# Performance work log

Measured on AMD Instinct MI355X. Metric: run time of the kernel, lower is better.

Reference implementation:

```python
import jax, jax.numpy as jnp
import numpy as np

H = 16          # num_heads
TOP_K = 2
LN_EPS = 1e-5


def setup_inputs() -> dict:
    key = jax.random.key(0)
    ks = jax.random.split(key, 8)
    B, S, E, NE = 2, 1024, 1024, 8
    w = lambda k, shp: jax.random.normal(k, shp, dtype=jnp.float32) * 0.02
    return {
        "x": jax.random.normal(ks[0], (B, S, E), dtype=jnp.float32),
        "rW1": w(ks[1], (E // 2, E)),
        "rb1": jnp.zeros((E // 2,), jnp.float32),
        "ln_g": jnp.ones((E // 2,), jnp.float32),
        "ln_b": jnp.zeros((E // 2,), jnp.float32),
        "rW2": w(ks[2], (NE, E // 2)),
        "rb2": jnp.zeros((NE,), jnp.float32),
        "qW": w(ks[3], (NE, E, E)),
        "qb": jnp.zeros((NE, E), jnp.float32),
        "kW": w(ks[4], (NE, E, E)),
        "kb": jnp.zeros((NE, E), jnp.float32),
        "vW": w(ks[5], (NE, E, E)),
        "vb": jnp.zeros((NE, E), jnp.float32),
        "oW": w(ks[6], (NE, E, E)),
        "ob": jnp.zeros((NE, E), jnp.float32),
    }


def reference(x, rW1, rb1, ln_g, ln_b, rW2, rb2, qW, qb, kW, kb, vW, vb, oW, ob):
    B, S, E = x.shape
    NE = qW.shape[0]
    Dh = E // H
    scale = 1.0 / jnp.sqrt(jnp.asarray(Dh, x.dtype))

    # ---- router: Linear -> LayerNorm -> ReLU -> Linear ----
    h = x @ rW1.T + rb1                       # [B,S,E/2]
    mu = h.mean(-1, keepdims=True)
    var = ((h - mu) ** 2).mean(-1, keepdims=True)
    h = (h - mu) * jax.lax.rsqrt(var + LN_EPS) * ln_g + ln_b
    h = jax.nn.relu(h)
    logits = h @ rW2.T + rb2                  # [B,S,NE]
    probs = jax.nn.softmax(logits, axis=-1)

    # ---- top-k gating, renormalized, scattered to dense expert mask ----
    tp, ti = jax.lax.top_k(probs, TOP_K)      # [B,S,K]
    tp = tp / tp.sum(-1, keepdims=True)
    expert_mask = (jax.nn.one_hot(ti, NE, dtype=probs.dtype) * tp[..., None]).sum(-2)  # [B,S,NE]
    gates = jnp.moveaxis(expert_mask, -1, 0)  # [NE,B,S]

    # ---- every expert attends over all tokens; outputs gated and summed ----
    def expert_step(acc, params):
        qw, qb_, kw, kb_, vw, vb_, ow, ob_, g = params
        q = (x @ qw.T + qb_).reshape(B, S, H, Dh).transpose(0, 2, 1, 3)  # [B,H,S,Dh]
        k = (x @ kw.T + kb_).reshape(B, S, H, Dh).transpose(0, 2, 1, 3)
        v = (x @ vw.T + vb_).reshape(B, S, H, Dh).transpose(0, 2, 1, 3)
        scores = jnp.einsum("bhqd,bhkd->bhqk", q, k) * scale
        p = jax.nn.softmax(scores, axis=-1)
        o = jnp.einsum("bhqk,bhkd->bhqd", p, v)
        o = o.transpose(0, 2, 1, 3).reshape(B, S, E) @ ow.T + ob_
        return acc + o * g[..., None], None

    out, _ = jax.lax.scan(expert_step, jnp.zeros_like(x),
                          (qW, qb, kW, kb, vW, vb, oW, ob, gates))
    return out
```

## Files before the change

### kernel.cpp

```cpp
#include <hip/hip_runtime.h>
#include <hip/hip_bf16.h>

typedef unsigned short u16;
typedef unsigned int u32;
typedef __bf16 bf16x8 __attribute__((ext_vector_type(8)));
typedef float f32x4 __attribute__((ext_vector_type(4)));

__device__ __forceinline__ u16 f2bf(float f) {
  union { float f; unsigned u; } v; v.f = f;
  unsigned r = v.u + 0x7fffu + ((v.u >> 16) & 1u);
  return (u16)(r >> 16);
}

__device__ __forceinline__ f32x4 mfma16(bf16x8 a, bf16x8 b, f32x4 c) {
  return __builtin_amdgcn_mfma_f32_16x16x32_bf16(a, b, c, 0, 0, 0);
}

__device__ __forceinline__ void gl_lds16(const u16* g, u16* l) {
  __builtin_amdgcn_global_load_lds(
      (const __attribute__((address_space(1))) u32*)g,
      (__attribute__((address_space(3))) u32*)l, 16, 0, 0);
}

__global__ __launch_bounds__(256) void cvt_x_kernel(const float* __restrict__ x, u16* __restrict__ xb) {
  size_t i = (size_t)blockIdx.x * 256 + threadIdx.x;
  float4 v = reinterpret_cast<const float4*>(x)[i];
  unsigned long long pk = (unsigned long long)f2bf(v.x) |
                          ((unsigned long long)f2bf(v.y) << 16) |
                          ((unsigned long long)f2bf(v.z) << 32) |
                          ((unsigned long long)f2bf(v.w) << 48);
  *reinterpret_cast<unsigned long long*>(xb + i * 4) = pk;
}

__global__ __launch_bounds__(256) void cvt_w_kernel(
    const float* __restrict__ qW, const float* __restrict__ kW,
    const float* __restrict__ vW, const float* __restrict__ oW,
    u16* __restrict__ wb_qkv, u16* __restrict__ wb_o) {
  const size_t nqkv4 = (size_t)8 * 3 * 262144;
  const size_t total = nqkv4 + (size_t)8 * 262144;
  for (size_t i = (size_t)blockIdx.x * 256 + threadIdx.x; i < total;
       i += (size_t)gridDim.x * 256) {
    const float* src; u16* dst;
    if (i < nqkv4) {
      size_t elem = i * 4;
      size_t blk = elem >> 20;
      size_t el = blk / 3, ty = blk % 3;
      const float* W = (ty == 0 ? qW : (ty == 1 ? kW : vW));
      src = W + el * 1048576 + (elem & 1048575);
      dst = wb_qkv + elem;
    } else {
      size_t elem = (i - nqkv4) * 4;
      size_t el = elem >> 20;
      src = oW + el * 1048576 + (elem & 1048575);
      dst = wb_o + elem;
    }
    float4 v = *reinterpret_cast<const float4*>(src);
    unsigned long long pk = (unsigned long long)f2bf(v.x) |
                            ((unsigned long long)f2bf(v.y) << 16) |
                            ((unsigned long long)f2bf(v.z) << 32) |
                            ((unsigned long long)f2bf(v.w) << 48);
    *reinterpret_cast<unsigned long long*>(dst) = pk;
  }
}

__global__ __launch_bounds__(256) void zero_lists(u32* __restrict__ lists) {
  int i = blockIdx.x * 256 + threadIdx.x;
  if (i < 32784) lists[i] = 0;
}

__global__ __launch_bounds__(256) void router_gemm1(
    const float* __restrict__ x, const float* __restrict__ rW1,
    const float* __restrict__ rb1, float* __restrict__ hbuf) {
  __shared__ float aT[16][72];
  __shared__ float bT[16][72];
  int t = threadIdx.x;
  int tx = t & 15, ty = t >> 4;
  int m0 = blockIdx.x * 64, n0 = blockIdx.y * 64;
  float acc[4][4];
#pragma unroll
  for (int i = 0; i < 4; ++i)
#pragma unroll
    for (int j = 0; j < 4; ++j) acc[i][j] = 0.f;
  const float* Ab = x + (size_t)m0 * 1024;
  const float* Bb = rW1 + (size_t)n0 * 1024;
  int r = t >> 2, c4 = (t & 3) * 4;
  for (int k0 = 0; k0 < 1024; k0 += 16) {
    float4 av = *reinterpret_cast<const float4*>(Ab + (size_t)r * 1024 + k0 + c4);
    float4 bv = *reinterpret_cast<const float4*>(Bb + (size_t)r * 1024 + k0 + c4);
    aT[c4 + 0][r] = av.x; aT[c4 + 1][r] = av.y; aT[c4 + 2][r] = av.z; aT[c4 + 3][r] = av.w;
    bT[c4 + 0][r] = bv.x; bT[c4 + 1][r] = bv.y; bT[c4 + 2][r] = bv.z; bT[c4 + 3][r] = bv.w;
    __syncthreads();
#pragma unroll
    for (int kk = 0; kk < 16; ++kk) {
      float4 a = *reinterpret_cast<const float4*>(&aT[kk][ty * 4]);
      float4 b = *reinterpret_cast<const float4*>(&bT[kk][tx * 4]);
      float aa[4] = {a.x, a.y, a.z, a.w};
      float bb[4] = {b.x, b.y, b.z, b.w};
#pragma unroll
      for (int i = 0; i < 4; ++i)
#pragma unroll
        for (int j = 0; j < 4; ++j) acc[i][j] += aa[i] * bb[j];
    }
    __syncthreads();
  }
#pragma unroll
  for (int i = 0; i < 4; ++i) {
    int row = m0 + ty * 4 + i;
#pragma unroll
    for (int j = 0; j < 4; ++j) {
      int col = n0 + tx * 4 + j;
      hbuf[(size_t)row * 512 + col] = acc[i][j] + rb1[col];
    }
  }
}

__global__ __launch_bounds__(64) void router_finish(
    const float* __restrict__ hbuf, const float* __restrict__ ln_g,
    const float* __restrict__ ln_b, const float* __restrict__ rW2,
    const float* __restrict__ rb2,
    u32* __restrict__ tok_list, float* __restrict__ gate_list,
    u32* __restrict__ cnt, u32* __restrict__ inv) {
  int tok = blockIdx.x, lane = threadIdx.x;
  const float* hr = hbuf + (size_t)tok * 512;
  float4 v0 = *reinterpret_cast<const float4*>(hr + lane * 8);
  float4 v1 = *reinterpret_cast<const float4*>(hr + lane * 8 + 4);
  float hv[8] = {v0.x, v0.y, v0.z, v0.w, v1.x, v1.y, v1.z, v1.w};
  float s = 0.f;
#pragma unroll
  for (int j = 0; j < 8; ++j) s += hv[j];
#pragma unroll
  for (int m = 1; m < 64; m <<= 1) s += __shfl_xor(s, m);
  float mu = s * (1.0f / 512.0f);
  float s2 = 0.f;
#pragma unroll
  for (int j = 0; j < 8; ++j) { float d = hv[j] - mu; s2 += d * d; }
#pragma unroll
  for (int m = 1; m < 64; m <<= 1) s2 += __shfl_xor(s2, m);
  float rstd = 1.0f / sqrtf(s2 * (1.0f / 512.0f) + 1e-5f);
#pragma unroll
  for (int j = 0; j < 8; ++j) {
    float tv = (hv[j] - mu) * rstd * ln_g[lane * 8 + j] + ln_b[lane * 8 + j];
    hv[j] = fmaxf(tv, 0.0f);
  }
  float logit[8];
#pragma unroll
  for (int n = 0; n < 8; ++n) {
    const float* wr = rW2 + (size_t)n * 512 + lane * 8;
    float p = 0.f;
#pragma unroll
    for (int j = 0; j < 8; ++j) p += hv[j] * wr[j];
#pragma unroll
    for (int m = 1; m < 64; m <<= 1) p += __shfl_xor(p, m);
    logit[n] = p + rb2[n];
  }
  int i1 = 0; float l1 = logit[0];
#pragma unroll
  for (int n = 1; n < 8; ++n) if (logit[n] > l1) { l1 = logit[n]; i1 = n; }
  int i2 = -1; float l2 = -3.4e38f;
#pragma unroll
  for (int n = 0; n < 8; ++n) if (n != i1 && logit[n] > l2) { l2 = logit[n]; i2 = n; }
  float e2 = __expf(l2 - l1);
  float g1 = 1.0f / (1.0f + e2);
  float g2 = e2 * g1;
  if (lane == 0) {
    int b = tok >> 10, sq = tok & 1023;
    int p1 = i1 * 2 + b;
    u32 pos1 = atomicAdd(&cnt[p1], 1u);
    tok_list[p1 * 1024 + pos1] = (u32)sq;
    gate_list[p1 * 1024 + pos1] = g1;
    inv[tok * 2 + 0] = ((u32)p1 << 10) | pos1;
    int p2 = i2 * 2 + b;
    u32 pos2 = atomicAdd(&cnt[p2], 1u);
    tok_list[p2 * 1024 + pos2] = (u32)sq;
    gate_list[p2 * 1024 + pos2] = g2;
    inv[tok * 2 + 1] = ((u32)p2 << 10) | pos2;
  }
}

__device__ __forceinline__ void stage8(
    const u16* aS0, const u16* aS1, const u16* aS2, const u16* aS3,
    const u16* bS0, const u16* bS1, const u16* bS2, const u16* bS3,
    int k0, u16* aL, u16* bL, int w) {
  gl_lds16(aS0 + k0, aL + (32 * w + 0) * 64);
  gl_lds16(aS1 + k0, aL + (32 * w + 8) * 64);
  gl_lds16(aS2 + k0, aL + (32 * w + 16) * 64);
  gl_lds16(aS3 + k0, aL + (32 * w + 24) * 64);
  gl_lds16(bS0 + k0, bL + (32 * w + 0) * 64);
  gl_lds16(bS1 + k0, bL + (32 * w + 8) * 64);
  gl_lds16(bS2 + k0, bL + (32 * w + 16) * 64);
  gl_lds16(bS3 + k0, bL + (32 * w + 24) * 64);
}

__device__ __forceinline__ void gemm_mainloop_p(
    const u16* aS0, const u16* aS1, const u16* aS2, const u16* aS3,
    const u16* bS0, const u16* bS1, const u16* bS2, const u16* bS3,
    int K, u16* aL0, u16* bL0, u16* aL1, u16* bL1, f32x4 acc[4][4]) {
  const int t = threadIdx.x;
  const int w = t >> 6, lane = t & 63;
  const int wm = (w >> 1) * 64, wn = (w & 1) * 64;
  const int lr = lane & 15, lg = lane >> 4;
  const int T = K >> 6;
  stage8(aS0, aS1, aS2, aS3, bS0, bS1, bS2, bS3, 0, aL0, bL0, w);
  __syncthreads();
  for (int tt = 0; tt < T; ++tt) {
    u16* aC = (tt & 1) ? aL1 : aL0;
    u16* bC = (tt & 1) ? bL1 : bL0;
    if (tt + 1 < T) {
      u16* aN = (tt & 1) ? aL0 : aL1;
      u16* bN = (tt & 1) ? bL0 : bL1;
      stage8(aS0, aS1, aS2, aS3, bS0, bS1, bS2, bS3, (tt + 1) << 6, aN, bN, w);
    }
    __builtin_amdgcn_s_setprio(1);
#pragma unroll
    for (int kk = 0; kk < 2; ++kk) {
      bf16x8 af[4], bfr[4];
#pragma unroll
      for (int i = 0; i < 4; ++i) {
        int ra = wm + i * 16 + lr;
        af[i] = *reinterpret_cast<const bf16x8*>(aC + ra * 64 + (((kk * 4 + lg) ^ (ra & 7)) << 3));
        int rb = wn + i * 16 + lr;
        bfr[i] = *reinterpret_cast<const bf16x8*>(bC + rb * 64 + (((kk * 4 + lg) ^ (rb & 7)) << 3));
      }
#pragma unroll
      for (int mi = 0; mi < 4; ++mi)
#pragma unroll
        for (int ni = 0; ni < 4; ++ni)
          acc[mi][ni] = mfma16(af[mi], bfr[ni], acc[mi][ni]);
    }
    __builtin_amdgcn_s_setprio(0);
    __syncthreads();
  }
}

__global__ __launch_bounds__(256) void kv_gemm_kernel(
    const u16* __restrict__ xb, const u16* __restrict__ wb_qkv,
    const float* __restrict__ kb, const float* __restrict__ vb,
    u16* __restrict__ kvbuf) {
  __shared__ u16 lds[32768];
  int orig = blockIdx.x;
  int wgid = (orig & 7) * 256 + (orig >> 3);
  int nblk = wgid & 7, mblk = (wgid >> 3) & 15;
  int ty = (wgid >> 7) & 1, e = wgid >> 8;
  const int t = threadIdx.x, w = t >> 6, lane = t & 63;
  const int rloc = lane >> 3, cloc = lane & 7;
  const int sc8 = (cloc ^ rloc) * 8;
  const u16* A = xb + (size_t)mblk * 128 * 1024;
  const u16* B = wb_qkv + (size_t)(e * 3 + 1 + ty) * 1048576 + (size_t)nblk * 128 * 1024;
  f32x4 acc[4][4];
#pragma unroll
  for (int i = 0; i < 4; ++i)
#pragma unroll
    for (int j = 0; j < 4; ++j) { f32x4 z = {0.f, 0.f, 0.f, 0.f}; acc[i][j] = z; }
  gemm_mainloop_p(
      A + (size_t)(32 * w + 0 + rloc) * 1024 + sc8, A + (size_t)(32 * w + 8 + rloc) * 1024 + sc8,
      A + (size_t)(32 * w + 16 + rloc) * 1024 + sc8, A + (size_t)(32 * w + 24 + rloc) * 1024 + sc8,
      B + (size_t)(32 * w + 0 + rloc) * 1024 + sc8, B + (size_t)(32 * w + 8 + rloc) * 1024 + sc8,
      B + (size_t)(32 * w + 16 + rloc) * 1024 + sc8, B + (size_t)(32 * w + 24 + rloc) * 1024 + sc8,
      1024, lds, lds + 8192, lds + 16384, lds + 24576, acc);
  const int wm = (w >> 1) * 64, wn = (w & 1) * 64;
  const int lr = lane & 15, lg = lane >> 4;
  const float* bias = (ty ? vb : kb) + (size_t)e * 1024 + nblk * 128;
  u16* Cb = kvbuf + ((size_t)(e * 2 + ty) * 2048 + (size_t)mblk * 128) * 1024 + nblk * 128;
#pragma unroll
  for (int ni = 0; ni < 4; ++ni) {
    int lcol = wn + ni * 16 + lr;
    float bv = bias[lcol];
#pragma unroll
    for (int mi = 0; mi < 4; ++mi)
#pragma unroll
      for (int rg = 0; rg < 4; ++rg) {
        int lrow = wm + mi * 16 + lg * 4 + rg;
        Cb[(size_t)lrow * 1024 + lcol] = f2bf(acc[mi][ni][rg] + bv);
      }
  }
}

__global__ __launch_bounds__(256) void q_gemm_kernel(
    const u16* __restrict__ xb, const u16* __restrict__ wb_qkv,
    const float* __restrict__ qb, const u32* __restrict__ tok_list,
    const u32* __restrict__ cnt, u16* __restrict__ qc) {
  __shared__ u16 lds[32768];
  int nblk = blockIdx.x, mt = blockIdx.y, p = blockIdx.z;
  int c = (int)cnt[p];
  if (mt * 128 >= c) return;
  int e = p >> 1, b = p & 1;
  const int t = threadIdx.x, w = t >> 6, lane = t & 63;
  const int rloc = lane >> 3, cloc = lane & 7;
  const int sc8 = (cloc ^ rloc) * 8;
  const u32* tl = tok_list + p * 1024 + mt * 128 + 32 * w + rloc;
  int t0 = (int)(tl[0] & 1023), t1 = (int)(tl[8] & 1023);
  int t2 = (int)(tl[16] & 1023), t3 = (int)(tl[24] & 1023);
  const u16* Ab = xb + (size_t)b * 1024 * 1024 + sc8;
  const u16* B = wb_qkv + (size_t)(e * 3) * 1048576 + (size_t)nblk * 128 * 1024;
  f32x4 acc[4][4];
#pragma unroll
  for (int i = 0; i < 4; ++i)
#pragma unroll
    for (int j = 0; j < 4; ++j) { f32x4 z = {0.f, 0.f, 0.f, 0.f}; acc[i][j] = z; }
  gemm_mainloop_p(
      Ab + (size_t)t0 * 1024, Ab + (size_t)t1 * 1024, Ab + (size_t)t2 * 1024, Ab + (size_t)t3 * 1024,
      B + (size_t)(32 * w + 0 + rloc) * 1024 + sc8, B + (size_t)(32 * w + 8 + rloc) * 1024 + sc8,
      B + (size_t)(32 * w + 16 + rloc) * 1024 + sc8, B + (size_t)(32 * w + 24 + rloc) * 1024 + sc8,
      1024, lds, lds + 8192, lds + 16384, lds + 24576, acc);
  const int wm = (w >> 1) * 64, wn = (w & 1) * 64;
  const int lr = lane & 15, lg = lane >> 4;
  const float* bias = qb + (size_t)e * 1024 + nblk * 128;
  u16* Cb = qc + ((size_t)p * 1024 + (size_t)mt * 128) * 1024 + nblk * 128;
#pragma unroll
  for (int ni = 0; ni < 4; ++ni) {
    int lcol = wn + ni * 16 + lr;
    float bv = bias[lcol];
#pragma unroll
    for (int mi = 0; mi < 4; ++mi)
#pragma unroll
      for (int rg = 0; rg < 4; ++rg) {
        int lrow = wm + mi * 16 + lg * 4 + rg;
        Cb[(size_t)lrow * 1024 + lcol] = f2bf(acc[mi][ni][rg] + bv);
      }
  }
}

__global__ __launch_bounds__(256) void attn_kernel(
    const u16* __restrict__ qc, const u16* __restrict__ kvbuf,
    const u32* __restrict__ cnt, u16* __restrict__ oc) {
  __shared__ u16 Kl[4096];
  __shared__ u32 Vtl[2048];
  __shared__ u16 Pl[4096];
  int h = blockIdx.x;
  int p = blockIdx.y >> 3, lt = blockIdx.y & 7;
  int c = (int)cnt[p];
  if (lt * 64 >= c) return;
  int e = p >> 1, b = p & 1;
  const u16* Qb = qc + ((size_t)p * 1024 + (size_t)lt * 64) * 1024 + h * 64;
  const u16* Kg = kvbuf + ((size_t)(e * 2 + 0) * 2048 + (size_t)b * 1024) * 1024 + h * 64;
  const u16* Vg = kvbuf + ((size_t)(e * 2 + 1) * 2048 + (size_t)b * 1024) * 1024 + h * 64;
  u16* Og = oc + ((size_t)p * 1024 + (size_t)lt * 64) * 1024 + h * 64;
  const int t = threadIdx.x, w = t >> 6, lane = t & 63;
  const int lr = lane & 15, lg = lane >> 4;
  const int krow_l = lane >> 3, kc = lane & 7;
  const int s2 = t >> 3, sc3 = t & 7;

  bf16x8 qa0 = *reinterpret_cast<const bf16x8*>(Qb + (size_t)(w * 16 + lr) * 1024 + lg * 8);
  bf16x8 qa1 = *reinterpret_cast<const bf16x8*>(Qb + (size_t)(w * 16 + lr) * 1024 + 32 + lg * 8);

  f32x4 oacc[4];
  float mrun[4], lsum[4];
#pragma unroll
  for (int i = 0; i < 4; ++i) {
    f32x4 z = {0.f, 0.f, 0.f, 0.f}; oacc[i] = z; mrun[i] = -3.4e38f; lsum[i] = 0.f;
  }

  for (int it = 0; it < 16; ++it) {
    int kv0 = it * 64;
#pragma unroll
    for (int r = 0; r < 2; ++r) {
      int row = 16 * w + 8 * r + krow_l;
      gl_lds16(Kg + (size_t)(kv0 + row) * 1024 + (kc ^ (row & 7)) * 8,
               Kl + (16 * w + 8 * r) * 64);
    }
    {
      int4 v0r = *reinterpret_cast<const int4*>(Vg + (size_t)(kv0 + 2 * s2) * 1024 + sc3 * 8);
      int4 v1r = *reinterpret_cast<const int4*>(Vg + (size_t)(kv0 + 2 * s2 + 1) * 1024 + sc3 * 8);
      const u16* v0 = reinterpret_cast<const u16*>(&v0r);
      const u16* v1 = reinterpret_cast<const u16*>(&v1r);
#pragma unroll
      for (int j = 0; j < 8; ++j) {
        int jj = (j + sc3) & 7;
        int d = sc3 * 8 + jj;
        u32 val = (u32)v0[jj] | ((u32)v1[jj] << 16);
        Vtl[d * 32 + (((s2 >> 2) ^ (d & 7)) << 2) + (s2 & 3)] = val;
      }
    }
    __syncthreads();
    f32x4 sv[4];
    __builtin_amdgcn_s_setprio(1);
#pragma unroll
    for (int nt = 0; nt < 4; ++nt) {
      f32x4 z = {0.f, 0.f, 0.f, 0.f};
#pragma unroll
      for (int kk = 0; kk < 2; ++kk) {
        int rk = nt * 16 + lr;
        bf16x8 kf = *reinterpret_cast<const bf16x8*>(Kl + rk * 64 + (((kk * 4 + lg) ^ (rk & 7)) << 3));
        z = mfma16(kk ? qa1 : qa0, kf, z);
      }
      sv[nt] = z * 0.125f;
    }
    __builtin_amdgcn_s_setprio(0);
#pragma unroll
    for (int rg = 0; rg < 4; ++rg) {
      float tm = fmaxf(fmaxf(sv[0][rg], sv[1][rg]), fmaxf(sv[2][rg], sv[3][rg]));
#pragma unroll
      for (int mm = 1; mm < 16; mm <<= 1) tm = fmaxf(tm, __shfl_xor(tm, mm));
      float mn = fmaxf(mrun[rg], tm);
      float al = __expf(mrun[rg] - mn);
      mrun[rg] = mn;
      lsum[rg] *= al;
#pragma unroll
      for (int nt = 0; nt < 4; ++nt) oacc[nt][rg] *= al;
    }
#pragma unroll
    for (int nt = 0; nt < 4; ++nt) {
#pragma unroll
      for (int rg = 0; rg < 4; ++rg) {
        float pv = __expf(sv[nt][rg] - mrun[rg]);
        lsum[rg] += pv;
        int prow = lg * 4 + rg;
        Pl[w * 1024 + prow * 64 + ((nt * 16 + lr) ^ ((prow & 7) << 3))] = f2bf(pv);
      }
    }
    __builtin_amdgcn_s_setprio(1);
#pragma unroll
    for (int kk = 0; kk < 2; ++kk) {
      bf16x8 pf = *reinterpret_cast<const bf16x8*>(
          Pl + w * 1024 + lr * 64 + (((kk * 4 + lg) ^ (lr & 7)) << 3));
#pragma unroll
      for (int nt = 0; nt < 4; ++nt) {
        int rv = nt * 16 + lr;
        bf16x8 vf = *reinterpret_cast<const bf16x8*>(
            reinterpret_cast<const u16*>(Vtl) + rv * 64 + (((kk * 4 + lg) ^ (rv & 7)) << 3));
        oacc[nt] = mfma16(pf, vf, oacc[nt]);
      }
    }
    __builtin_amdgcn_s_setprio(0);
    __syncthreads();
  }
#pragma unroll
  for (int rg = 0; rg < 4; ++rg) {
#pragma unroll
    for (int mm = 1; mm < 16; mm <<= 1) lsum[rg] += __shfl_xor(lsum[rg], mm);
    float inv = 1.0f / lsum[rg];
#pragma unroll
    for (int nt = 0; nt < 4; ++nt)
      Og[(size_t)(w * 16 + lg * 4 + rg) * 1024 + nt * 16 + lr] = f2bf(oacc[nt][rg] * inv);
  }
}

__global__ __launch_bounds__(256) void oproj_kernel(
    const u16* __restrict__ oc, const u16* __restrict__ wb_o,
    const u32* __restrict__ cnt, float* __restrict__ projc) {
  __shared__ u16 lds[32768];
  int nblk = blockIdx.x, mt = blockIdx.y, p = blockIdx.z;
  int c = (int)cnt[p];
  if (mt * 128 >= c) return;
  int e = p >> 1;
  const int t = threadIdx.x, w = t >> 6, lane = t & 63;
  const int rloc = lane >> 3, cloc = lane & 7;
  const int sc8 = (cloc ^ rloc) * 8;
  const u16* A = oc + ((size_t)p * 1024 + (size_t)mt * 128) * 1024;
  const u16* B = wb_o + (size_t)e * 1048576 + (size_t)nblk * 128 * 1024;
  f32x4 acc[4][4];
#pragma unroll
  for (int i = 0; i < 4; ++i)
#pragma unroll
    for (int j = 0; j < 4; ++j) { f32x4 z = {0.f, 0.f, 0.f, 0.f}; acc[i][j] = z; }
  gemm_mainloop_p(
      A + (size_t)(32 * w + 0 + rloc) * 1024 + sc8, A + (size_t)(32 * w + 8 + rloc) * 1024 + sc8,
      A + (size_t)(32 * w + 16 + rloc) * 1024 + sc8, A + (size_t)(32 * w + 24 + rloc) * 1024 + sc8,
      B + (size_t)(32 * w + 0 + rloc) * 1024 + sc8, B + (size_t)(32 * w + 8 + rloc) * 1024 + sc8,
      B + (size_t)(32 * w + 16 + rloc) * 1024 + sc8, B + (size_t)(32 * w + 24 + rloc) * 1024 + sc8,
      1024, lds, lds + 8192, lds + 16384, lds + 24576, acc);
  const int wm = (w >> 1) * 64, wn = (w & 1) * 64;
  const int lr = lane & 15, lg = lane >> 4;
  float* Pb = projc + ((size_t)p * 1024 + (size_t)mt * 128) * 1024 + nblk * 128;
#pragma unroll
  for (int mi = 0; mi < 4; ++mi)
#pragma unroll
    for (int rg = 0; rg < 4; ++rg) {
      int lrow = wm + mi * 16 + lg * 4 + rg;
#pragma unroll
      for (int ni = 0; ni < 4; ++ni) {
        int lcol = wn + ni * 16 + lr;
        Pb[(size_t)lrow * 1024 + lcol] = acc[mi][ni][rg];
      }
    }
}

__global__ __launch_bounds__(256) void merge_out(
    const float* __restrict__ projc, const float* __restrict__ ob,
    const float* __restrict__ gate_list, const u32* __restrict__ inv,
    float* __restrict__ out) {
  int tok = blockIdx.x;
  int c4 = threadIdx.x * 4;
  u32 i1 = inv[tok * 2], i2 = inv[tok * 2 + 1];
  int idx1 = (int)(i1 >> 10) * 1024 + (int)(i1 & 1023);
  int idx2 = (int)(i2 >> 10) * 1024 + (int)(i2 & 1023);
  float g1 = gate_list[idx1], g2 = gate_list[idx2];
  int e1 = (int)(i1 >> 11), e2 = (int)(i2 >> 11);
  float4 a = *reinterpret_cast<const float4*>(projc + (size_t)idx1 * 1024 + c4);
  float4 bvec = *reinterpret_cast<const float4*>(projc + (size_t)idx2 * 1024 + c4);
  float4 o1 = *reinterpret_cast<const float4*>(ob + (size_t)e1 * 1024 + c4);
  float4 o2 = *reinterpret_cast<const float4*>(ob + (size_t)e2 * 1024 + c4);
  float4 r;
  r.x = g1 * (a.x + o1.x) + g2 * (bvec.x + o2.x);
  r.y = g1 * (a.y + o1.y) + g2 * (bvec.y + o2.y);
  r.z = g1 * (a.z + o1.z) + g2 * (bvec.z + o2.z);
  r.w = g1 * (a.w + o1.w) + g2 * (bvec.w + o2.w);
  *reinterpret_cast<float4*>(out + (size_t)tok * 1024 + c4) = r;
}

extern "C" void kernel_launch(void* const* d_in, const int* in_sizes, int n_in,
                              void* d_out, int out_size, void* d_ws, size_t ws_size,
                              hipStream_t stream) {
  const float* x    = (const float*)d_in[0];
  const float* rW1  = (const float*)d_in[1];
  const float* rb1  = (const float*)d_in[2];
  const float* ln_g = (const float*)d_in[3];
  const float* ln_b = (const float*)d_in[4];
  const float* rW2  = (const float*)d_in[5];
  const float* rb2  = (const float*)d_in[6];
  const float* qW   = (const float*)d_in[7];
  const float* qb   = (const float*)d_in[8];
  const float* kW   = (const float*)d_in[9];
  const float* kb   = (const float*)d_in[10];
  const float* vW   = (const float*)d_in[11];
  const float* vb   = (const float*)d_in[12];
  const float* oW   = (const float*)d_in[13];
  const float* ob   = (const float*)d_in[14];
  float* out = (float*)d_out;

  const size_t need = 50331648ull + 16777216ull + 67108864ull + 33554432ull +
                      33554432ull + 4194304ull + 147520ull;
  if (ws_size < need) return;
  char* pp = (char*)d_ws;
  u16* wb_qkv = (u16*)pp; pp += 50331648ull;
  u16* wb_o   = (u16*)pp; pp += 16777216ull;
  u16* kvbuf  = (u16*)pp; pp += 67108864ull;
  u16* qc     = (u16*)pp; pp += 33554432ull;
  u16* oc     = (u16*)pp; pp += 33554432ull;
  u16* xb     = (u16*)pp; pp += 4194304ull;
  u32* lists  = (u32*)pp;
  u32* tok_list    = lists;
  float* gate_list = (float*)(lists + 16384);
  u32* cnt         = lists + 32768;
  u32* inv         = lists + 32784;
  float* hbuf  = (float*)qc;
  float* projc = (float*)kvbuf;

  cvt_x_kernel<<<dim3(2048), dim3(256), 0, stream>>>(x, xb);
  cvt_w_kernel<<<dim3(2048), dim3(256), 0, stream>>>(qW, kW, vW, oW, wb_qkv, wb_o);
  router_gemm1<<<dim3(32, 8), dim3(256), 0, stream>>>(x, rW1, rb1, hbuf);
  zero_lists<<<dim3(129), dim3(256), 0, stream>>>(lists);
  router_finish<<<dim3(2048), dim3(64), 0, stream>>>(hbuf, ln_g, ln_b, rW2, rb2,
                                                     tok_list, gate_list, cnt, inv);
  kv_gemm_kernel<<<dim3(2048), dim3(256), 0, stream>>>(xb, wb_qkv, kb, vb, kvbuf);
  q_gemm_kernel<<<dim3(8, 8, 16), dim3(256), 0, stream>>>(xb, wb_qkv, qb, tok_list, cnt, qc);
  attn_kernel<<<dim3(16, 128), dim3(256), 0, stream>>>(qc, kvbuf, cnt, oc);
  oproj_kernel<<<dim3(8, 8, 16), dim3(256), 0, stream>>>(oc, wb_o, cnt, projc);
  merge_out<<<dim3(2048), dim3(256), 0, stream>>>(projc, ob, gate_list, inv, out);
}
```

Before: 539.5 us.

## Emit transposed V from the KV GEMM and double-buffer K/V tiles in attention

The V projection GEMM now swaps its operands (weight times x) so it writes V already transposed per expert and batch into a separate buffer. K also moves to its own buffer. The attention kernel can then stage both K and V^T tiles with direct global-to-LDS loads, instead of doing register-level V transposes with scattered LDS stores. It also double-buffers these tiles, prefetching the next KV block while computing the current one. The cost is twice the K/V LDS footprint, a per-row bias lookup in the V epilogue, and reliance on the existing end-of-loop barrier to order the async LDS loads.

Result: faster. 485.3 us (-10.0%).

```diff
diff --git a/kernel.cpp b/kernel.cpp
--- a/kernel.cpp
+++ b/kernel.cpp
@@ -235,17 +235,26 @@
 __global__ __launch_bounds__(256) void kv_gemm_kernel(
     const u16* __restrict__ xb, const u16* __restrict__ wb_qkv,
     const float* __restrict__ kb, const float* __restrict__ vb,
-    u16* __restrict__ kvbuf) {
+    u16* __restrict__ kbuf, u16* __restrict__ vtbuf) {
   __shared__ u16 lds[32768];
   int orig = blockIdx.x;
   int wgid = (orig & 7) * 256 + (orig >> 3);
-  int nblk = wgid & 7, mblk = (wgid >> 3) & 15;
-  int ty = (wgid >> 7) & 1, e = wgid >> 8;
+  int e = wgid >> 8, r = wgid & 255;
+  int ty = r >> 7, rr = r & 127;
   const int t = threadIdx.x, w = t >> 6, lane = t & 63;
   const int rloc = lane >> 3, cloc = lane & 7;
   const int sc8 = (cloc ^ rloc) * 8;
-  const u16* A = xb + (size_t)mblk * 128 * 1024;
-  const u16* B = wb_qkv + (size_t)(e * 3 + 1 + ty) * 1048576 + (size_t)nblk * 128 * 1024;
+  const u16 *A, *B;
+  int mblk, nblk;
+  if (ty == 0) {
+    mblk = rr >> 3; nblk = rr & 7;
+    A = xb + (size_t)mblk * 128 * 1024;
+    B = wb_qkv + (size_t)(e * 3 + 1) * 1048576 + (size_t)nblk * 128 * 1024;
+  } else {
+    mblk = rr & 7; nblk = rr >> 3;
+    A = wb_qkv + (size_t)(e * 3 + 2) * 1048576 + (size_t)mblk * 128 * 1024;
+    B = xb + (size_t)nblk * 128 * 1024;
+  }
   f32x4 acc[4][4];
 #pragma unroll
   for (int i = 0; i < 4; ++i)
@@ -259,19 +268,36 @@
       1024, lds, lds + 8192, lds + 16384, lds + 24576, acc);
   const int wm = (w >> 1) * 64, wn = (w & 1) * 64;
   const int lr = lane & 15, lg = lane >> 4;
-  const float* bias = (ty ? vb : kb) + (size_t)e * 1024 + nblk * 128;
-  u16* Cb = kvbuf + ((size_t)(e * 2 + ty) * 2048 + (size_t)mblk * 128) * 1024 + nblk * 128;
-#pragma unroll
-  for (int ni = 0; ni < 4; ++ni) {
-    int lcol = wn + ni * 16 + lr;
-    float bv = bias[lcol];
-#pragma unroll
-    for (int mi = 0; mi < 4; ++mi)
-#pragma unroll
-      for (int rg = 0; rg < 4; ++rg) {
-        int lrow = wm + mi * 16 + lg * 4 + rg;
-        Cb[(size_t)lrow * 1024 + lcol] = f2bf(acc[mi][ni][rg] + bv);
-      }
+  if (ty == 0) {
+    const float* bias = kb + (size_t)e * 1024 + nblk * 128;
+    u16* Cb = kbuf + ((size_t)e * 2048 + (size_t)mblk * 128) * 1024 + nblk * 128;
+#pragma unroll
+    for (int ni = 0; ni < 4; ++ni) {
+      int lcol = wn + ni * 16 + lr;
+      float bv = bias[lcol];
+#pragma unroll
+      for (int mi = 0; mi < 4; ++mi)
+#pragma unroll
+        for (int rg = 0; rg < 4; ++rg) {
+          int lrow = wm + mi * 16 + lg * 4 + rg;
+          Cb[(size_t)lrow * 1024 + lcol] = f2bf(acc[mi][ni][rg] + bv);
+        }
+    }
+  } else {
+    const float* bias = vb + (size_t)e * 1024 + mblk * 128;
+    int bb = nblk >> 3, nn = nblk & 7;
+    u16* Cb = vtbuf + ((size_t)(e * 2 + bb) * 1024 + (size_t)mblk * 128) * 1024 + nn * 128;
+#pragma unroll
+    for (int ni = 0; ni < 4; ++ni) {
+      int lcol = wn + ni * 16 + lr;
+#pragma unroll
+      for (int mi = 0; mi < 4; ++mi)
+#pragma unroll
+        for (int rg = 0; rg < 4; ++rg) {
+          int lrow = wm + mi * 16 + lg * 4 + rg;
+          Cb[(size_t)lrow * 1024 + lcol] = f2bf(acc[mi][ni][rg] + bias[lrow]);
+        }
+    }
   }
 }
 
@@ -321,10 +347,11 @@
 }
 
 __global__ __launch_bounds__(256) void attn_kernel(
-    const u16* __restrict__ qc, const u16* __restrict__ kvbuf,
-    const u32* __restrict__ cnt, u16* __restrict__ oc) {
-  __shared__ u16 Kl[4096];
-  __shared__ u32 Vtl[2048];
+    const u16* __restrict__ qc, const u16* __restrict__ kbuf,
+    const u16* __restrict__ vtbuf, const u32* __restrict__ cnt,
+    u16* __restrict__ oc) {
+  __shared__ u16 Kl[2][4096];
+  __shared__ u16 Vtl[2][4096];
   __shared__ u16 Pl[4096];
   int h = blockIdx.x;
   int p = blockIdx.y >> 3, lt = blockIdx.y & 7;
@@ -332,13 +359,27 @@
   if (lt * 64 >= c) return;
   int e = p >> 1, b = p & 1;
   const u16* Qb = qc + ((size_t)p * 1024 + (size_t)lt * 64) * 1024 + h * 64;
-  const u16* Kg = kvbuf + ((size_t)(e * 2 + 0) * 2048 + (size_t)b * 1024) * 1024 + h * 64;
-  const u16* Vg = kvbuf + ((size_t)(e * 2 + 1) * 2048 + (size_t)b * 1024) * 1024 + h * 64;
+  const u16* Kg = kbuf + ((size_t)e * 2048 + (size_t)b * 1024) * 1024 + h * 64;
+  const u16* Vtg = vtbuf + ((size_t)(e * 2 + b) * 1024 + (size_t)h * 64) * 1024;
   u16* Og = oc + ((size_t)p * 1024 + (size_t)lt * 64) * 1024 + h * 64;
   const int t = threadIdx.x, w = t >> 6, lane = t & 63;
   const int lr = lane & 15, lg = lane >> 4;
-  const int krow_l = lane >> 3, kc = lane & 7;
-  const int s2 = t >> 3, sc3 = t & 7;
+  const int rloc = lane >> 3, kc = lane & 7;
+
+#define STAGE_ATTN(IT, KB, VB)                                                   \
+  {                                                                              \
+    int kv0_ = (IT) * 64;                                                        \
+    _Pragma("unroll")                                                            \
+    for (int r_ = 0; r_ < 2; ++r_) {                                             \
+      int row_ = 16 * w + 8 * r_ + rloc;                                         \
+      gl_lds16(Kg + (size_t)(kv0_ + row_) * 1024 + (kc ^ (row_ & 7)) * 8,        \
+               (KB) + (16 * w + 8 * r_) * 64);                                   \
+      gl_lds16(Vtg + (size_t)row_ * 1024 + kv0_ + (kc ^ (row_ & 7)) * 8,         \
+               (VB) + (16 * w + 8 * r_) * 64);                                   \
+    }                                                                            \
+  }
+
+  STAGE_ATTN(0, Kl[0], Vtl[0]);
 
   bf16x8 qa0 = *reinterpret_cast<const bf16x8*>(Qb + (size_t)(w * 16 + lr) * 1024 + lg * 8);
   bf16x8 qa1 = *reinterpret_cast<const bf16x8*>(Qb + (size_t)(w * 16 + lr) * 1024 + 32 + lg * 8);
@@ -349,29 +390,13 @@
   for (int i = 0; i < 4; ++i) {
     f32x4 z = {0.f, 0.f, 0.f, 0.f}; oacc[i] = z; mrun[i] = -3.4e38f; lsum[i] = 0.f;
   }
+  __syncthreads();
 
   for (int it = 0; it < 16; ++it) {
-    int kv0 = it * 64;
-#pragma unroll
-    for (int r = 0; r < 2; ++r) {
-      int row = 16 * w + 8 * r + krow_l;
-      gl_lds16(Kg + (size_t)(kv0 + row) * 1024 + (kc ^ (row & 7)) * 8,
-               Kl + (16 * w + 8 * r) * 64);
-    }
-    {
-      int4 v0r = *reinterpret_cast<const int4*>(Vg + (size_t)(kv0 + 2 * s2) * 1024 + sc3 * 8);
-      int4 v1r = *reinterpret_cast<const int4*>(Vg + (size_t)(kv0 + 2 * s2 + 1) * 1024 + sc3 * 8);
-      const u16* v0 = reinterpret_cast<const u16*>(&v0r);
-      const u16* v1 = reinterpret_cast<const u16*>(&v1r);
-#pragma unroll
-      for (int j = 0; j < 8; ++j) {
-        int jj = (j + sc3) & 7;
-        int d = sc3 * 8 + jj;
-        u32 val = (u32)v0[jj] | ((u32)v1[jj] << 16);
-        Vtl[d * 32 + (((s2 >> 2) ^ (d & 7)) << 2) + (s2 & 3)] = val;
-      }
-    }
-    __syncthreads();
+    const int cur = it & 1;
+    const u16* Kc = Kl[cur];
+    const u16* Vc = Vtl[cur];
+    if (it + 1 < 16) STAGE_ATTN(it + 1, Kl[cur ^ 1], Vtl[cur ^ 1]);
     f32x4 sv[4];
     __builtin_amdgcn_s_setprio(1);
 #pragma unroll
@@ -380,7 +405,7 @@
 #pragma unroll
       for (int kk = 0; kk < 2; ++kk) {
         int rk = nt * 16 + lr;
-        bf16x8 kf = *reinterpret_cast<const bf16x8*>(Kl + rk * 64 + (((kk * 4 + lg) ^ (rk & 7)) << 3));
+        bf16x8 kf = *reinterpret_cast<const bf16x8*>(Kc + rk * 64 + (((kk * 4 + lg) ^ (rk & 7)) << 3));
         z = mfma16(kk ? qa1 : qa0, kf, z);
       }
       sv[nt] = z * 0.125f;
@@ -416,8 +441,7 @@
 #pragma unroll
       for (int nt = 0; nt < 4; ++nt) {
         int rv = nt * 16 + lr;
-        bf16x8 vf = *reinterpret_cast<const bf16x8*>(
-            reinterpret_cast<const u16*>(Vtl) + rv * 64 + (((kk * 4 + lg) ^ (rv & 7)) << 3));
+        bf16x8 vf = *reinterpret_cast<const bf16x8*>(Vc + rv * 64 + (((kk * 4 + lg) ^ (rv & 7)) << 3));
         oacc[nt] = mfma16(pf, vf, oacc[nt]);
       }
     }
@@ -433,6 +457,7 @@
     for (int nt = 0; nt < 4; ++nt)
       Og[(size_t)(w * 16 + lg * 4 + rg) * 1024 + nt * 16 + lr] = f2bf(oacc[nt][rg] * inv);
   }
+#undef STAGE_ATTN
 }
 
 __global__ __launch_bounds__(256) void oproj_kernel(
@@ -524,7 +549,8 @@
   char* pp = (char*)d_ws;
   u16* wb_qkv = (u16*)pp; pp += 50331648ull;
   u16* wb_o   = (u16*)pp; pp += 16777216ull;
-  u16* kvbuf  = (u16*)pp; pp += 67108864ull;
+  u16* kbuf   = (u16*)pp; pp += 33554432ull;
+  u16* vtbuf  = (u16*)pp; pp += 33554432ull;
   u16* qc     = (u16*)pp; pp += 33554432ull;
   u16* oc     = (u16*)pp; pp += 33554432ull;
   u16* xb     = (u16*)pp; pp += 4194304ull;
@@ -534,7 +560,7 @@
   u32* cnt         = lists + 32768;
   u32* inv         = lists + 32784;
   float* hbuf  = (float*)qc;
-  float* projc = (float*)kvbuf;
+  float* projc = (float*)kbuf;
 
   cvt_x_kernel<<<dim3(2048), dim3(256), 0, stream>>>(x, xb);
   cvt_w_kernel<<<dim3(2048), dim3(256), 0, stream>>>(qW, kW, vW, oW, wb_qkv, wb_o);
@@ -542,9 +568,9 @@
   zero_lists<<<dim3(129), dim3(256), 0, stream>>>(lists);
   router_finish<<<dim3(2048), dim3(64), 0, stream>>>(hbuf, ln_g, ln_b, rW2, rb2,
                                                      tok_list, gate_list, cnt, inv);
-  kv_gemm_kernel<<<dim3(2048), dim3(256), 0, stream>>>(xb, wb_qkv, kb, vb, kvbuf);
+  kv_gemm_kernel<<<dim3(2048), dim3(256), 0, stream>>>(xb, wb_qkv, kb, vb, kbuf, vtbuf);
   q_gemm_kernel<<<dim3(8, 8, 16), dim3(256), 0, stream>>>(xb, wb_qkv, qb, tok_list, cnt, qc);
-  attn_kernel<<<dim3(16, 128), dim3(256), 0, stream>>>(qc, kvbuf, cnt, oc);
+  attn_kernel<<<dim3(16, 128), dim3(256), 0, stream>>>(qc, kbuf, vtbuf, cnt, oc);
   oproj_kernel<<<dim3(8, 8, 16), dim3(256), 0, stream>>>(oc, wb_o, cnt, projc);
   merge_out<<<dim3(2048), dim3(256), 0, stream>>>(projc, ob, gate_list, inv, out);
 }
```
